# Kernel optimization log

Measured on AMD Instinct MI355X. Metric: run time of the kernel, lower is better.

The kernel has to match this reference:

```python
import jax, jax.numpy as jnp
import numpy as np

B, S, D, H = 2, 2048, 1024, 16
DK = D // H


def setup_inputs() -> dict:
    key = jax.random.key(0)
    ks = jax.random.split(key, 12)
    scale = 1.0 / np.sqrt(D)
    inp = {
        "Q": jax.random.normal(ks[0], (B, S, D), jnp.float32),
        "K": jax.random.normal(ks[1], (B, S, D), jnp.float32),
        "V": jax.random.normal(ks[2], (B, S, D), jnp.float32),
        # causal mask, broadcast over batch: [B, S, S]
        "mask": jnp.broadcast_to(jnp.tril(jnp.ones((S, S), jnp.bool_)), (B, S, S)),
        "WQ_w": jax.random.normal(ks[3], (D, D), jnp.float32) * scale,
        "WQ_b": jnp.zeros((D,), jnp.float32),
        "WK_w": jax.random.normal(ks[4], (D, D), jnp.float32) * scale,
        "WK_b": jnp.zeros((D,), jnp.float32),
        "WV_w": jax.random.normal(ks[5], (D, D), jnp.float32) * scale,
        "WV_b": jnp.zeros((D,), jnp.float32),
        "WO_w": jax.random.normal(ks[6], (D, D), jnp.float32) * scale,
        "WO_b": jnp.zeros((D,), jnp.float32),
    }
    return inp


def reference(Q, K, V, mask, WQ_w, WQ_b, WK_w, WK_b, WV_w, WV_b, WO_w, WO_b):
    # Linear projections (torch Linear: x @ W.T + b), split heads -> [B,H,S,DK]
    def proj(x, w, b):
        return (x @ w.T + b).reshape(B, S, H, DK).transpose(0, 2, 1, 3)

    q = proj(Q, WQ_w, WQ_b)
    k = proj(K, WK_w, WK_b)
    v = proj(V, WV_w, WV_b)

    scores = jnp.einsum("bhqd,bhkd->bhqk", q, k) / jnp.sqrt(jnp.asarray(DK, q.dtype))
    scores = jnp.where(mask[:, None, :, :], scores, -jnp.inf)
    attn = jax.nn.softmax(scores, axis=-1)  # dropout is identity in eval mode

    out = jnp.einsum("bhqk,bhkd->bhqd", attn, v)
    out = out.transpose(0, 2, 1, 3).reshape(B, S, D)
    out = out @ WO_w.T + WO_b
    return (out, attn)
```

## Files before the change

### kernel.cpp

```cpp
#include <hip/hip_runtime.h>

#define S_LEN 2048
#define DMODEL 1024
#define NHEAD 16
#define DKH 64
#define BATCH 2

typedef __bf16 bf16_t;
typedef __bf16 bf16x8 __attribute__((ext_vector_type(8)));
typedef __bf16 bf16x4 __attribute__((ext_vector_type(4)));
typedef float f32x4 __attribute__((ext_vector_type(4)));

__device__ __forceinline__ void gload16(const bf16_t* g, bf16_t* l) {
  __builtin_amdgcn_global_load_lds(
      (const __attribute__((address_space(1))) unsigned int*)g,
      (__attribute__((address_space(3))) unsigned int*)l,
      16, 0, 0);
}

__global__ void cvt_all(const float* __restrict__ Q, const float* __restrict__ K,
                        const float* __restrict__ V, const float* __restrict__ WQ,
                        const float* __restrict__ WK, const float* __restrict__ WV,
                        const float* __restrict__ WO, bf16_t* __restrict__ dst) {
  const int i = blockIdx.x * 256 + threadIdx.x;
  const float* src;
  int off;
  if (i < 1572864) {
    const int seg = i >> 19;
    off = i & 524287;
    src = (seg == 0) ? Q : ((seg == 1) ? K : V);
  } else {
    const int j = i - 1572864;
    const int seg = j >> 17;
    off = j & 131071;
    src = (seg == 0) ? WQ : ((seg == 1) ? WK : ((seg == 2) ? WV : WO));
  }
  f32x4 a = *(const f32x4*)(src + (size_t)off * 8);
  f32x4 b = *(const f32x4*)(src + (size_t)off * 8 + 4);
  bf16x8 v;
#pragma unroll
  for (int j = 0; j < 4; ++j) { v[j] = (bf16_t)a[j]; v[4 + j] = (bf16_t)b[j]; }
  *(bf16x8*)(dst + (size_t)i * 8) = v;
}

struct GOp {
  const bf16_t* A;
  const bf16_t* W;
  const float* bias;
  char* out;
  int emode;
};

#define GM 4096
#define GN 1024
#define GK 1024
#define BM 128
#define BN 128
#define BK 64

__launch_bounds__(256, 3)
__global__ void gemm_bf16(GOp op0, GOp op1, GOp op2) {
  GOp op = (blockIdx.z == 0) ? op0 : ((blockIdx.z == 1) ? op1 : op2);
  const int n0 = blockIdx.x * BN;
  const int m0 = blockIdx.y * BM;
  const int t = threadIdx.x;
  const int w = t >> 6;
  const int l = t & 63;
  const int wr = w >> 1, wc = w & 1;
  const int lg = l >> 4, ll = l & 15;
  const int sr = l >> 3;
  const int sc = l & 7;

  __shared__ __align__(16) bf16_t Asm[BM * BK];
  __shared__ __align__(16) bf16_t Bsm[BM * BK];

  f32x4 acc[4][4] = {};

  for (int kt = 0; kt < GK / BK; ++kt) {
    __syncthreads();
#pragma unroll
    for (int i = 0; i < 4; ++i) {
      const int rbase = i * 32 + (w << 3);
      const int row = rbase + sr;
      const int gc = (sc ^ (row & 7)) << 3;
      gload16(op.A + (size_t)(m0 + row) * GK + kt * BK + gc, &Asm[rbase * BK]);
      gload16(op.W + (size_t)(n0 + row) * GK + kt * BK + gc, &Bsm[rbase * BK]);
    }
    __syncthreads();

    bf16x8 af[4][2], bfr[4][2];
#pragma unroll
    for (int mi = 0; mi < 4; ++mi) {
      const int row = wr * 64 + mi * 16 + ll;
      af[mi][0] = *(const bf16x8*)&Asm[row * BK + ((lg ^ (row & 7)) << 3)];
      af[mi][1] = *(const bf16x8*)&Asm[row * BK + (((4 + lg) ^ (row & 7)) << 3)];
    }
#pragma unroll
    for (int ni = 0; ni < 4; ++ni) {
      const int row = wc * 64 + ni * 16 + ll;
      bfr[ni][0] = *(const bf16x8*)&Bsm[row * BK + ((lg ^ (row & 7)) << 3)];
      bfr[ni][1] = *(const bf16x8*)&Bsm[row * BK + (((4 + lg) ^ (row & 7)) << 3)];
    }
#pragma unroll
    for (int mi = 0; mi < 4; ++mi)
#pragma unroll
      for (int ni = 0; ni < 4; ++ni) {
        acc[mi][ni] = __builtin_amdgcn_mfma_f32_16x16x32_bf16(af[mi][0], bfr[ni][0], acc[mi][ni], 0, 0, 0);
        acc[mi][ni] = __builtin_amdgcn_mfma_f32_16x16x32_bf16(af[mi][1], bfr[ni][1], acc[mi][ni], 0, 0, 0);
      }
  }

#pragma unroll
  for (int mi = 0; mi < 4; ++mi) {
#pragma unroll
    for (int ni = 0; ni < 4; ++ni) {
      const int col = n0 + wc * 64 + ni * 16 + ll;
      const int rbase = m0 + wr * 64 + mi * 16 + (lg << 2);
      const float bval = op.bias[col];
      f32x4 v = acc[mi][ni];
      if (op.emode == 0) {
        bf16_t* o = (bf16_t*)op.out;
#pragma unroll
        for (int r = 0; r < 4; ++r)
          o[(size_t)(rbase + r) * GN + col] = (bf16_t)(v[r] + bval);
      } else {
        const int hh = col >> 6, dd = col & 63;
        const int bb = rbase >> 11, ss = rbase & (S_LEN - 1);
        bf16_t* o = (bf16_t*)op.out + (((size_t)bb * NHEAD + hh) * DKH + dd) * S_LEN + ss;
        bf16x4 pk;
#pragma unroll
        for (int r = 0; r < 4; ++r) pk[r] = (bf16_t)(v[r] + bval);
        *(bf16x4*)o = pk;
      }
    }
  }
}

__launch_bounds__(256, 4)
__global__ void gemm_out64(const bf16_t* __restrict__ A, const bf16_t* __restrict__ W,
                           const float* __restrict__ bias, float* __restrict__ out) {
  const int n0 = blockIdx.x * 128;
  const int m0 = blockIdx.y * 64;
  const int t = threadIdx.x;
  const int w = t >> 6;
  const int l = t & 63;
  const int wr = w >> 1, wc = w & 1;
  const int lg = l >> 4, ll = l & 15;
  const int sr = l >> 3;
  const int sc = l & 7;

  __shared__ __align__(16) bf16_t Asm[64 * BK];
  __shared__ __align__(16) bf16_t Bsm[128 * BK];

  f32x4 acc[2][4] = {};

  for (int kt = 0; kt < GK / BK; ++kt) {
    __syncthreads();
    {
#pragma unroll
      for (int i = 0; i < 2; ++i) {
        const int rbase = i * 32 + (w << 3);
        const int row = rbase + sr;
        const int gc = (sc ^ (row & 7)) << 3;
        gload16(A + (size_t)(m0 + row) * GK + kt * BK + gc, &Asm[rbase * BK]);
      }
#pragma unroll
      for (int i = 0; i < 4; ++i) {
        const int rbase = i * 32 + (w << 3);
        const int row = rbase + sr;
        const int gc = (sc ^ (row & 7)) << 3;
        gload16(W + (size_t)(n0 + row) * GK + kt * BK + gc, &Bsm[rbase * BK]);
      }
    }
    __syncthreads();

    bf16x8 af[2][2], bfr[4][2];
#pragma unroll
    for (int mi = 0; mi < 2; ++mi) {
      const int row = wr * 32 + mi * 16 + ll;
      af[mi][0] = *(const bf16x8*)&Asm[row * BK + ((lg ^ (row & 7)) << 3)];
      af[mi][1] = *(const bf16x8*)&Asm[row * BK + (((4 + lg) ^ (row & 7)) << 3)];
    }
#pragma unroll
    for (int ni = 0; ni < 4; ++ni) {
      const int row = wc * 64 + ni * 16 + ll;
      bfr[ni][0] = *(const bf16x8*)&Bsm[row * BK + ((lg ^ (row & 7)) << 3)];
      bfr[ni][1] = *(const bf16x8*)&Bsm[row * BK + (((4 + lg) ^ (row & 7)) << 3)];
    }
#pragma unroll
    for (int mi = 0; mi < 2; ++mi)
#pragma unroll
      for (int ni = 0; ni < 4; ++ni) {
        acc[mi][ni] = __builtin_amdgcn_mfma_f32_16x16x32_bf16(af[mi][0], bfr[ni][0], acc[mi][ni], 0, 0, 0);
        acc[mi][ni] = __builtin_amdgcn_mfma_f32_16x16x32_bf16(af[mi][1], bfr[ni][1], acc[mi][ni], 0, 0, 0);
      }
  }

#pragma unroll
  for (int mi = 0; mi < 2; ++mi) {
#pragma unroll
    for (int ni = 0; ni < 4; ++ni) {
      const int col = n0 + wc * 64 + ni * 16 + ll;
      const int rbase = m0 + wr * 32 + mi * 16 + (lg << 2);
      const float bval = bias[col];
      f32x4 v = acc[mi][ni];
#pragma unroll
      for (int r = 0; r < 4; ++r)
        out[(size_t)(rbase + r) * GN + col] = v[r] + bval;
    }
  }
}

__launch_bounds__(256, 2)
__global__ void attn2(const bf16_t* __restrict__ qp, const bf16_t* __restrict__ kp,
                      const bf16_t* __restrict__ vT, float* __restrict__ attn_out,
                      bf16_t* __restrict__ ctx) {
  const int raw = blockIdx.x;
  const int wg = (raw & 7) * 64 + (raw >> 3);
  const int bh = wg >> 4;
  const int pr = wg & 15;
  const int b = bh >> 4, h = bh & 15;
  const int flip = (raw >> 8) & 1;

  __shared__ __align__(16) bf16_t Qs[64 * 64];
  __shared__ __align__(16) bf16_t Ks[2][128 * 64];
  __shared__ __align__(16) bf16_t Vs[2][2][64 * 64];
  __shared__ __align__(16) bf16_t Pt[4][16 * 64];
  float* rinvS = (float*)&Pt[0][0];

  const int t = threadIdx.x;
  const int w = t >> 6;
  const int l = t & 63;
  const int lg = l >> 4;
  const int ll = l & 15;
  const int sr = l >> 3;
  const int sc = l & 7;

  const bf16_t* kbh = kp + (size_t)b * S_LEN * DMODEL + h * DKH;
  const bf16_t* vbh = vT + (size_t)bh * DKH * S_LEN;

#define KV_STAGE128(bu, ktt)                                                              \
  {                                                                                       \
    _Pragma("unroll") for (int i = 0; i < 4; ++i) {                                       \
      const int rbase = i * 32 + (w << 3);                                                \
      const int row = rbase + sr;                                                         \
      const int gc = (sc ^ (row & 7)) << 3;                                               \
      gload16(kbh + (size_t)((ktt) * 128 + row) * DMODEL + gc, &Ks[bu][rbase * 64]);      \
    }                                                                                     \
    _Pragma("unroll") for (int i = 0; i < 2; ++i) {                                       \
      const int rbase = i * 32 + (w << 3);                                                \
      const int row = rbase + sr;                                                         \
      const int gc = (sc ^ (row & 7)) << 3;                                               \
      gload16(vbh + (size_t)row * S_LEN + (ktt) * 128 + gc, &Vs[bu][0][rbase * 64]);      \
      gload16(vbh + (size_t)row * S_LEN + (ktt) * 128 + 64 + gc, &Vs[bu][1][rbase * 64]); \
    }                                                                                     \
  }

#define K_STAGE(bu, kt)                                                            \
  {                                                                                \
    _Pragma("unroll") for (int i = 0; i < 2; ++i) {                                \
      const int rbase = i * 32 + (w << 3);                                         \
      const int row = rbase + sr;                                                  \
      const int gc = (sc ^ (row & 7)) << 3;                                        \
      gload16(kbh + (size_t)((kt) * 64 + row) * DMODEL + gc, &Ks[bu][rbase * 64]); \
    }                                                                              \
  }

  for (int half = 0; half < 2; ++half) {
    const int qt = (half ^ flip) ? (31 - pr) : pr;
    const int q0 = qt * 64;
    const int nktt = (qt + 2) >> 1;

    __syncthreads();
#pragma unroll
    for (int i = 0; i < 2; ++i) {
      const int rbase = i * 32 + (w << 3);
      const int row = rbase + sr;
      const int gc = (sc ^ (row & 7)) << 3;
      gload16(qp + (size_t)(b * S_LEN + q0 + row) * DMODEL + h * DKH + gc, &Qs[rbase * 64]);
    }
    KV_STAGE128(0, 0);
    __syncthreads();

    bf16x8 qf0, qf1;
    {
      const int row = w * 16 + ll;
      qf0 = *(const bf16x8*)&Qs[row * 64 + ((lg ^ (row & 7)) << 3)];
      qf1 = *(const bf16x8*)&Qs[row * 64 + (((4 + lg) ^ (row & 7)) << 3)];
    }

    f32x4 oacc[4] = {};
    float sums[4] = {0.f, 0.f, 0.f, 0.f};
    const int qrow_base = q0 + w * 16 + (lg << 2);

    int cur = 0;
    for (int ktt = 0; ktt < nktt; ++ktt) {
      if (ktt + 1 < nktt) KV_STAGE128(cur ^ 1, ktt + 1);

      __builtin_amdgcn_s_setprio(1);
#pragma unroll
      for (int s = 0; s < 2; ++s) {
        const int kk = 2 * ktt + s;
        if (kk <= qt) {
          const bool diag = (kk == qt);
#pragma unroll
          for (int cb = 0; cb < 4; ++cb) {
            const int lr = s * 64 + cb * 16 + ll;
            bf16x8 kf0 = *(const bf16x8*)&Ks[cur][lr * 64 + ((lg ^ (lr & 7)) << 3)];
            bf16x8 kf1 = *(const bf16x8*)&Ks[cur][lr * 64 + (((4 + lg) ^ (lr & 7)) << 3)];
            f32x4 a = {0.f, 0.f, 0.f, 0.f};
            a = __builtin_amdgcn_mfma_f32_16x16x32_bf16(qf0, kf0, a, 0, 0, 0);
            a = __builtin_amdgcn_mfma_f32_16x16x32_bf16(qf1, kf1, a, 0, 0, 0);
            const int gcol = kk * 64 + cb * 16 + ll;
            if (diag) {
#pragma unroll
              for (int r = 0; r < 4; ++r) {
                const float e = (gcol <= qrow_base + r) ? __expf(a[r] * 0.125f) : 0.0f;
                sums[r] += e;
                const int ql = (lg << 2) + r;
                const int k = cb * 16 + ll;
                *(bf16_t*)((char*)&Pt[w][0] + ql * 128 + (((k >> 3) ^ (ql & 7)) << 4) + ((k & 7) << 1)) = (bf16_t)e;
              }
            } else {
#pragma unroll
              for (int r = 0; r < 4; ++r) {
                const float e = __expf(a[r] * 0.125f);
                sums[r] += e;
                const int ql = (lg << 2) + r;
                const int k = cb * 16 + ll;
                *(bf16_t*)((char*)&Pt[w][0] + ql * 128 + (((k >> 3) ^ (ql & 7)) << 4) + ((k & 7) << 1)) = (bf16_t)e;
              }
            }
          }
          bf16x8 pa0 = *(const bf16x8*)((char*)&Pt[w][0] + ll * 128 + ((lg ^ (ll & 7)) << 4));
          bf16x8 pa1 = *(const bf16x8*)((char*)&Pt[w][0] + ll * 128 + (((4 + lg) ^ (ll & 7)) << 4));
#pragma unroll
          for (int db = 0; db < 4; ++db) {
            const int drow = db * 16 + ll;
            bf16x8 vf0 = *(const bf16x8*)&Vs[cur][s][drow * 64 + ((lg ^ (drow & 7)) << 3)];
            bf16x8 vf1 = *(const bf16x8*)&Vs[cur][s][drow * 64 + (((4 + lg) ^ (drow & 7)) << 3)];
            oacc[db] = __builtin_amdgcn_mfma_f32_16x16x32_bf16(pa0, vf0, oacc[db], 0, 0, 0);
            oacc[db] = __builtin_amdgcn_mfma_f32_16x16x32_bf16(pa1, vf1, oacc[db], 0, 0, 0);
          }
        }
      }
      __builtin_amdgcn_s_setprio(0);
      __syncthreads();
      cur ^= 1;
    }

    float rinv[4];
#pragma unroll
    for (int r = 0; r < 4; ++r) {
      float s = sums[r];
      s += __shfl_xor(s, 1);
      s += __shfl_xor(s, 2);
      s += __shfl_xor(s, 4);
      s += __shfl_xor(s, 8);
      rinv[r] = 1.0f / s;
    }
    if (ll == 0) {
#pragma unroll
      for (int r = 0; r < 4; ++r) rinvS[w * 16 + (lg << 2) + r] = rinv[r];
    }

    K_STAGE(0, 0);

#pragma unroll
    for (int db = 0; db < 4; ++db)
#pragma unroll
      for (int r = 0; r < 4; ++r) {
        const int grow = q0 + w * 16 + (lg << 2) + r;
        ctx[(size_t)(b * S_LEN + grow) * DMODEL + h * DKH + db * 16 + ll] = (bf16_t)(oacc[db][r] * rinv[r]);
      }
    __syncthreads();

    const float rv = rinvS[w * 16 + ll];
    float* arow = attn_out + ((size_t)bh * S_LEN + q0) * S_LEN;

    for (int kt = qt + 1; kt < 32; ++kt) {
      f32x4 z = {0.f, 0.f, 0.f, 0.f};
#pragma unroll
      for (int j = 0; j < 4; ++j) {
        const int row = w * 16 + (lg << 2) + j;
        *(f32x4*)(arow + (size_t)row * S_LEN + kt * 64 + (ll << 2)) = z;
      }
    }

    const int qrow_sw = q0 + w * 16 + ll;
    int cur2 = 0;
    for (int kt = 0; kt <= qt; ++kt) {
      if (kt + 1 <= qt) K_STAGE(cur2 ^ 1, kt + 1);

      const bool diag = (kt == qt);
#pragma unroll
      for (int i = 0; i < 4; ++i) {
        const int krow = i * 16 + ll;
        bf16x8 kf0 = *(const bf16x8*)&Ks[cur2][krow * 64 + ((lg ^ (krow & 7)) << 3)];
        bf16x8 kf1 = *(const bf16x8*)&Ks[cur2][krow * 64 + (((4 + lg) ^ (krow & 7)) << 3)];
        f32x4 a = {0.f, 0.f, 0.f, 0.f};
        a = __builtin_amdgcn_mfma_f32_16x16x32_bf16(kf0, qf0, a, 0, 0, 0);
        a = __builtin_amdgcn_mfma_f32_16x16x32_bf16(kf1, qf1, a, 0, 0, 0);
        const int kbase = kt * 64 + i * 16 + (lg << 2);
        f32x4 o;
        if (diag) {
#pragma unroll
          for (int r = 0; r < 4; ++r)
            o[r] = (kbase + r <= qrow_sw) ? __expf(a[r] * 0.125f) * rv : 0.0f;
        } else {
#pragma unroll
          for (int r = 0; r < 4; ++r) o[r] = __expf(a[r] * 0.125f) * rv;
        }
        *(f32x4*)(arow + (size_t)(w * 16 + ll) * S_LEN + kbase) = o;
      }
      __syncthreads();
      cur2 ^= 1;
    }
  }
#undef KV_STAGE128
#undef K_STAGE
}

extern "C" void kernel_launch(void* const* d_in, const int* in_sizes, int n_in,
                              void* d_out, int out_size, void* d_ws, size_t ws_size,
                              hipStream_t stream) {
  const float* Q   = (const float*)d_in[0];
  const float* K   = (const float*)d_in[1];
  const float* V   = (const float*)d_in[2];
  const float* WQw = (const float*)d_in[4];
  const float* WQb = (const float*)d_in[5];
  const float* WKw = (const float*)d_in[6];
  const float* WKb = (const float*)d_in[7];
  const float* WVw = (const float*)d_in[8];
  const float* WVb = (const float*)d_in[9];
  const float* WOw = (const float*)d_in[10];
  const float* WOb = (const float*)d_in[11];

  char* ws = (char*)d_ws;
  bf16_t* qb  = (bf16_t*)(ws);
  bf16_t* kb  = (bf16_t*)(ws + (size_t)( 8 << 20));
  bf16_t* vb  = (bf16_t*)(ws + (size_t)(16 << 20));
  bf16_t* wq  = (bf16_t*)(ws + (size_t)(24 << 20));
  bf16_t* wk  = (bf16_t*)(ws + (size_t)(26 << 20));
  bf16_t* wv  = (bf16_t*)(ws + (size_t)(28 << 20));
  bf16_t* wo  = (bf16_t*)(ws + (size_t)(30 << 20));
  bf16_t* qp  = (bf16_t*)(ws + (size_t)(32 << 20));
  bf16_t* kp  = (bf16_t*)(ws + (size_t)(40 << 20));
  bf16_t* vT  = (bf16_t*)(ws + (size_t)(48 << 20));
  bf16_t* ctx = (bf16_t*)(ws + (size_t)(56 << 20));

  float* out_main = (float*)d_out;
  float* attn_out = out_main + (size_t)BATCH * S_LEN * DMODEL;

  cvt_all<<<dim3(8192), 256, 0, stream>>>(Q, K, V, WQw, WKw, WVw, WOw, (bf16_t*)ws);

  GOp opq{qb, wq, WQb, (char*)qp, 0};
  GOp opk{kb, wk, WKb, (char*)kp, 0};
  GOp opv{vb, wv, WVb, (char*)vT, 1};
  gemm_bf16<<<dim3(8, 32, 3), 256, 0, stream>>>(opq, opk, opv);

  attn2<<<dim3(512), 256, 0, stream>>>(qp, kp, vT, attn_out, ctx);

  gemm_out64<<<dim3(8, 64), 256, 0, stream>>>(ctx, wo, WOb, out_main);
}
```

Before: 213.8 us.

## Split attention into one query tile per block with smaller LDS for higher occupancy

The attention kernel stops processing two paired query tiles per block and gives each block a single 64-row query tile, doubling the grid to 1024 blocks with a zigzag mapping across (b,h) for load balance. K/V staging shrinks from 128-key to 64-key tiles, and the P scratch reuses the Q shared buffer, cutting LDS so launch bounds can request 4 blocks per CU. The aim is more resident waves to hide latency and less tail imbalance. In exchange there are more barriers per key, Q is reloaded per block, and lower register budgets could cause spills.

```diff
diff --git a/kernel.cpp b/kernel.cpp
--- a/kernel.cpp
+++ b/kernel.cpp
@@ -156,21 +156,19 @@
 
   for (int kt = 0; kt < GK / BK; ++kt) {
     __syncthreads();
-    {
-#pragma unroll
-      for (int i = 0; i < 2; ++i) {
-        const int rbase = i * 32 + (w << 3);
-        const int row = rbase + sr;
-        const int gc = (sc ^ (row & 7)) << 3;
-        gload16(A + (size_t)(m0 + row) * GK + kt * BK + gc, &Asm[rbase * BK]);
-      }
-#pragma unroll
-      for (int i = 0; i < 4; ++i) {
-        const int rbase = i * 32 + (w << 3);
-        const int row = rbase + sr;
-        const int gc = (sc ^ (row & 7)) << 3;
-        gload16(W + (size_t)(n0 + row) * GK + kt * BK + gc, &Bsm[rbase * BK]);
-      }
+#pragma unroll
+    for (int i = 0; i < 2; ++i) {
+      const int rbase = i * 32 + (w << 3);
+      const int row = rbase + sr;
+      const int gc = (sc ^ (row & 7)) << 3;
+      gload16(A + (size_t)(m0 + row) * GK + kt * BK + gc, &Asm[rbase * BK]);
+    }
+#pragma unroll
+    for (int i = 0; i < 4; ++i) {
+      const int rbase = i * 32 + (w << 3);
+      const int row = rbase + sr;
+      const int gc = (sc ^ (row & 7)) << 3;
+      gload16(W + (size_t)(n0 + row) * GK + kt * BK + gc, &Bsm[rbase * BK]);
     }
     __syncthreads();
 
@@ -211,22 +209,23 @@
   }
 }
 
-__launch_bounds__(256, 2)
-__global__ void attn2(const bf16_t* __restrict__ qp, const bf16_t* __restrict__ kp,
+__launch_bounds__(256, 4)
+__global__ void attn4(const bf16_t* __restrict__ qp, const bf16_t* __restrict__ kp,
                       const bf16_t* __restrict__ vT, float* __restrict__ attn_out,
                       bf16_t* __restrict__ ctx) {
   const int raw = blockIdx.x;
-  const int wg = (raw & 7) * 64 + (raw >> 3);
-  const int bh = wg >> 4;
-  const int pr = wg & 15;
+  const int wg = (raw & 7) * 128 + (raw >> 3);
+  const int bh = wg >> 5;
+  const int i5 = wg & 31;
+  const int zig = (i5 & 1) ? (31 - (i5 >> 1)) : (i5 >> 1);
+  const int qt = (bh & 1) ? (31 - zig) : zig;
   const int b = bh >> 4, h = bh & 15;
-  const int flip = (raw >> 8) & 1;
+  const int q0 = qt * 64;
+  const int nkt = qt + 1;
 
   __shared__ __align__(16) bf16_t Qs[64 * 64];
-  __shared__ __align__(16) bf16_t Ks[2][128 * 64];
-  __shared__ __align__(16) bf16_t Vs[2][2][64 * 64];
-  __shared__ __align__(16) bf16_t Pt[4][16 * 64];
-  float* rinvS = (float*)&Pt[0][0];
+  __shared__ __align__(16) bf16_t Ks[2][64 * 64];
+  __shared__ __align__(16) bf16_t Vs[2][64 * 64];
 
   const int t = threadIdx.x;
   const int w = t >> 6;
@@ -236,188 +235,173 @@
   const int sr = l >> 3;
   const int sc = l & 7;
 
+  char* PtW = (char*)Qs + (w << 11);
+  float* rinvS = (float*)Qs;
+
   const bf16_t* kbh = kp + (size_t)b * S_LEN * DMODEL + h * DKH;
   const bf16_t* vbh = vT + (size_t)bh * DKH * S_LEN;
 
-#define KV_STAGE128(bu, ktt)                                                              \
-  {                                                                                       \
-    _Pragma("unroll") for (int i = 0; i < 4; ++i) {                                       \
-      const int rbase = i * 32 + (w << 3);                                                \
-      const int row = rbase + sr;                                                         \
-      const int gc = (sc ^ (row & 7)) << 3;                                               \
-      gload16(kbh + (size_t)((ktt) * 128 + row) * DMODEL + gc, &Ks[bu][rbase * 64]);      \
-    }                                                                                     \
-    _Pragma("unroll") for (int i = 0; i < 2; ++i) {                                       \
-      const int rbase = i * 32 + (w << 3);                                                \
-      const int row = rbase + sr;                                                         \
-      const int gc = (sc ^ (row & 7)) << 3;                                               \
-      gload16(vbh + (size_t)row * S_LEN + (ktt) * 128 + gc, &Vs[bu][0][rbase * 64]);      \
-      gload16(vbh + (size_t)row * S_LEN + (ktt) * 128 + 64 + gc, &Vs[bu][1][rbase * 64]); \
-    }                                                                                     \
-  }
-
-#define K_STAGE(bu, kt)                                                            \
-  {                                                                                \
-    _Pragma("unroll") for (int i = 0; i < 2; ++i) {                                \
-      const int rbase = i * 32 + (w << 3);                                         \
-      const int row = rbase + sr;                                                  \
-      const int gc = (sc ^ (row & 7)) << 3;                                        \
-      gload16(kbh + (size_t)((kt) * 64 + row) * DMODEL + gc, &Ks[bu][rbase * 64]); \
-    }                                                                              \
-  }
-
-  for (int half = 0; half < 2; ++half) {
-    const int qt = (half ^ flip) ? (31 - pr) : pr;
-    const int q0 = qt * 64;
-    const int nktt = (qt + 2) >> 1;
-
-    __syncthreads();
-#pragma unroll
-    for (int i = 0; i < 2; ++i) {
-      const int rbase = i * 32 + (w << 3);
-      const int row = rbase + sr;
-      const int gc = (sc ^ (row & 7)) << 3;
-      gload16(qp + (size_t)(b * S_LEN + q0 + row) * DMODEL + h * DKH + gc, &Qs[rbase * 64]);
-    }
-    KV_STAGE128(0, 0);
-    __syncthreads();
-
-    bf16x8 qf0, qf1;
-    {
-      const int row = w * 16 + ll;
-      qf0 = *(const bf16x8*)&Qs[row * 64 + ((lg ^ (row & 7)) << 3)];
-      qf1 = *(const bf16x8*)&Qs[row * 64 + (((4 + lg) ^ (row & 7)) << 3)];
-    }
-
-    f32x4 oacc[4] = {};
-    float sums[4] = {0.f, 0.f, 0.f, 0.f};
-    const int qrow_base = q0 + w * 16 + (lg << 2);
-
-    int cur = 0;
-    for (int ktt = 0; ktt < nktt; ++ktt) {
-      if (ktt + 1 < nktt) KV_STAGE128(cur ^ 1, ktt + 1);
-
-      __builtin_amdgcn_s_setprio(1);
-#pragma unroll
-      for (int s = 0; s < 2; ++s) {
-        const int kk = 2 * ktt + s;
-        if (kk <= qt) {
-          const bool diag = (kk == qt);
-#pragma unroll
-          for (int cb = 0; cb < 4; ++cb) {
-            const int lr = s * 64 + cb * 16 + ll;
-            bf16x8 kf0 = *(const bf16x8*)&Ks[cur][lr * 64 + ((lg ^ (lr & 7)) << 3)];
-            bf16x8 kf1 = *(const bf16x8*)&Ks[cur][lr * 64 + (((4 + lg) ^ (lr & 7)) << 3)];
-            f32x4 a = {0.f, 0.f, 0.f, 0.f};
-            a = __builtin_amdgcn_mfma_f32_16x16x32_bf16(qf0, kf0, a, 0, 0, 0);
-            a = __builtin_amdgcn_mfma_f32_16x16x32_bf16(qf1, kf1, a, 0, 0, 0);
-            const int gcol = kk * 64 + cb * 16 + ll;
-            if (diag) {
-#pragma unroll
-              for (int r = 0; r < 4; ++r) {
-                const float e = (gcol <= qrow_base + r) ? __expf(a[r] * 0.125f) : 0.0f;
-                sums[r] += e;
-                const int ql = (lg << 2) + r;
-                const int k = cb * 16 + ll;
-                *(bf16_t*)((char*)&Pt[w][0] + ql * 128 + (((k >> 3) ^ (ql & 7)) << 4) + ((k & 7) << 1)) = (bf16_t)e;
-              }
-            } else {
-#pragma unroll
-              for (int r = 0; r < 4; ++r) {
-                const float e = __expf(a[r] * 0.125f);
-                sums[r] += e;
-                const int ql = (lg << 2) + r;
-                const int k = cb * 16 + ll;
-                *(bf16_t*)((char*)&Pt[w][0] + ql * 128 + (((k >> 3) ^ (ql & 7)) << 4) + ((k & 7) << 1)) = (bf16_t)e;
-              }
-            }
-          }
-          bf16x8 pa0 = *(const bf16x8*)((char*)&Pt[w][0] + ll * 128 + ((lg ^ (ll & 7)) << 4));
-          bf16x8 pa1 = *(const bf16x8*)((char*)&Pt[w][0] + ll * 128 + (((4 + lg) ^ (ll & 7)) << 4));
-#pragma unroll
-          for (int db = 0; db < 4; ++db) {
-            const int drow = db * 16 + ll;
-            bf16x8 vf0 = *(const bf16x8*)&Vs[cur][s][drow * 64 + ((lg ^ (drow & 7)) << 3)];
-            bf16x8 vf1 = *(const bf16x8*)&Vs[cur][s][drow * 64 + (((4 + lg) ^ (drow & 7)) << 3)];
-            oacc[db] = __builtin_amdgcn_mfma_f32_16x16x32_bf16(pa0, vf0, oacc[db], 0, 0, 0);
-            oacc[db] = __builtin_amdgcn_mfma_f32_16x16x32_bf16(pa1, vf1, oacc[db], 0, 0, 0);
-          }
+#define KV_STAGE(bu, kt_)                                                           \
+  {                                                                                 \
+    _Pragma("unroll") for (int i = 0; i < 2; ++i) {                                 \
+      const int rbase = i * 32 + (w << 3);                                          \
+      const int row = rbase + sr;                                                   \
+      const int gc = (sc ^ (row & 7)) << 3;                                         \
+      gload16(kbh + (size_t)((kt_) * 64 + row) * DMODEL + gc, &Ks[bu][rbase * 64]); \
+      gload16(vbh + (size_t)row * S_LEN + (kt_) * 64 + gc, &Vs[bu][rbase * 64]);    \
+    }                                                                               \
+  }
+
+#define K_STAGE(bu, kt_)                                                            \
+  {                                                                                 \
+    _Pragma("unroll") for (int i = 0; i < 2; ++i) {                                 \
+      const int rbase = i * 32 + (w << 3);                                          \
+      const int row = rbase + sr;                                                   \
+      const int gc = (sc ^ (row & 7)) << 3;                                         \
+      gload16(kbh + (size_t)((kt_) * 64 + row) * DMODEL + gc, &Ks[bu][rbase * 64]); \
+    }                                                                               \
+  }
+
+#pragma unroll
+  for (int i = 0; i < 2; ++i) {
+    const int rbase = i * 32 + (w << 3);
+    const int row = rbase + sr;
+    const int gc = (sc ^ (row & 7)) << 3;
+    gload16(qp + (size_t)(b * S_LEN + q0 + row) * DMODEL + h * DKH + gc, &Qs[rbase * 64]);
+  }
+  KV_STAGE(0, 0);
+  __syncthreads();
+
+  bf16x8 qf0, qf1;
+  {
+    const int row = w * 16 + ll;
+    qf0 = *(const bf16x8*)&Qs[row * 64 + ((lg ^ (row & 7)) << 3)];
+    qf1 = *(const bf16x8*)&Qs[row * 64 + (((4 + lg) ^ (row & 7)) << 3)];
+  }
+  __syncthreads();
+
+  f32x4 oacc[4] = {};
+  float sums[4] = {0.f, 0.f, 0.f, 0.f};
+  const int qrow_base = q0 + w * 16 + (lg << 2);
+
+  int cur = 0;
+  for (int kt = 0; kt < nkt; ++kt) {
+    if (kt + 1 < nkt) KV_STAGE(cur ^ 1, kt + 1);
+
+    const bool diag = (kt == qt);
+    __builtin_amdgcn_s_setprio(1);
+#pragma unroll
+    for (int cb = 0; cb < 4; ++cb) {
+      const int krow = cb * 16 + ll;
+      bf16x8 kf0 = *(const bf16x8*)&Ks[cur][krow * 64 + ((lg ^ (krow & 7)) << 3)];
+      bf16x8 kf1 = *(const bf16x8*)&Ks[cur][krow * 64 + (((4 + lg) ^ (krow & 7)) << 3)];
+      f32x4 a = {0.f, 0.f, 0.f, 0.f};
+      a = __builtin_amdgcn_mfma_f32_16x16x32_bf16(qf0, kf0, a, 0, 0, 0);
+      a = __builtin_amdgcn_mfma_f32_16x16x32_bf16(qf1, kf1, a, 0, 0, 0);
+      const int gcol = kt * 64 + krow;
+      if (diag) {
+#pragma unroll
+        for (int r = 0; r < 4; ++r) {
+          const float e = (gcol <= qrow_base + r) ? __expf(a[r] * 0.125f) : 0.0f;
+          sums[r] += e;
+          const int ql = (lg << 2) + r;
+          const int k = cb * 16 + ll;
+          *(bf16_t*)(PtW + ql * 128 + (((k >> 3) ^ (ql & 7)) << 4) + ((k & 7) << 1)) = (bf16_t)e;
+        }
+      } else {
+#pragma unroll
+        for (int r = 0; r < 4; ++r) {
+          const float e = __expf(a[r] * 0.125f);
+          sums[r] += e;
+          const int ql = (lg << 2) + r;
+          const int k = cb * 16 + ll;
+          *(bf16_t*)(PtW + ql * 128 + (((k >> 3) ^ (ql & 7)) << 4) + ((k & 7) << 1)) = (bf16_t)e;
         }
       }
-      __builtin_amdgcn_s_setprio(0);
-      __syncthreads();
-      cur ^= 1;
-    }
-
-    float rinv[4];
+    }
+    bf16x8 pa0 = *(const bf16x8*)(PtW + ll * 128 + ((lg ^ (ll & 7)) << 4));
+    bf16x8 pa1 = *(const bf16x8*)(PtW + ll * 128 + (((4 + lg) ^ (ll & 7)) << 4));
+#pragma unroll
+    for (int db = 0; db < 4; ++db) {
+      const int drow = db * 16 + ll;
+      bf16x8 vf0 = *(const bf16x8*)&Vs[cur][drow * 64 + ((lg ^ (drow & 7)) << 3)];
+      bf16x8 vf1 = *(const bf16x8*)&Vs[cur][drow * 64 + (((4 + lg) ^ (drow & 7)) << 3)];
+      oacc[db] = __builtin_amdgcn_mfma_f32_16x16x32_bf16(pa0, vf0, oacc[db], 0, 0, 0);
+      oacc[db] = __builtin_amdgcn_mfma_f32_16x16x32_bf16(pa1, vf1, oacc[db], 0, 0, 0);
+    }
+    __builtin_amdgcn_s_setprio(0);
+    __syncthreads();
+    cur ^= 1;
+  }
+
+  float rinv[4];
+#pragma unroll
+  for (int r = 0; r < 4; ++r) {
+    float s = sums[r];
+    s += __shfl_xor(s, 1);
+    s += __shfl_xor(s, 2);
+    s += __shfl_xor(s, 4);
+    s += __shfl_xor(s, 8);
+    rinv[r] = 1.0f / s;
+  }
+  if (ll == 0) {
+#pragma unroll
+    for (int r = 0; r < 4; ++r) rinvS[w * 16 + (lg << 2) + r] = rinv[r];
+  }
+
+  K_STAGE(0, 0);
+
+#pragma unroll
+  for (int db = 0; db < 4; ++db)
 #pragma unroll
     for (int r = 0; r < 4; ++r) {
-      float s = sums[r];
-      s += __shfl_xor(s, 1);
-      s += __shfl_xor(s, 2);
-      s += __shfl_xor(s, 4);
-      s += __shfl_xor(s, 8);
-      rinv[r] = 1.0f / s;
-    }
-    if (ll == 0) {
-#pragma unroll
-      for (int r = 0; r < 4; ++r) rinvS[w * 16 + (lg << 2) + r] = rinv[r];
-    }
-
-    K_STAGE(0, 0);
-
-#pragma unroll
-    for (int db = 0; db < 4; ++db)
-#pragma unroll
-      for (int r = 0; r < 4; ++r) {
-        const int grow = q0 + w * 16 + (lg << 2) + r;
-        ctx[(size_t)(b * S_LEN + grow) * DMODEL + h * DKH + db * 16 + ll] = (bf16_t)(oacc[db][r] * rinv[r]);
+      const int grow = q0 + w * 16 + (lg << 2) + r;
+      ctx[(size_t)(b * S_LEN + grow) * DMODEL + h * DKH + db * 16 + ll] = (bf16_t)(oacc[db][r] * rinv[r]);
+    }
+  __syncthreads();
+
+  const float rv = rinvS[w * 16 + ll];
+  float* arow = attn_out + ((size_t)bh * S_LEN + q0) * S_LEN;
+
+  for (int kt = qt + 1; kt < 32; ++kt) {
+    f32x4 z = {0.f, 0.f, 0.f, 0.f};
+#pragma unroll
+    for (int j = 0; j < 4; ++j) {
+      const int row = w * 16 + (lg << 2) + j;
+      *(f32x4*)(arow + (size_t)row * S_LEN + kt * 64 + (ll << 2)) = z;
+    }
+  }
+
+  const int qrow_sw = q0 + w * 16 + ll;
+  int cur2 = 0;
+  for (int kt = 0; kt <= qt; ++kt) {
+    if (kt + 1 <= qt) K_STAGE(cur2 ^ 1, kt + 1);
+
+    const bool diag = (kt == qt);
+#pragma unroll
+    for (int i = 0; i < 4; ++i) {
+      const int krow = i * 16 + ll;
+      bf16x8 kf0 = *(const bf16x8*)&Ks[cur2][krow * 64 + ((lg ^ (krow & 7)) << 3)];
+      bf16x8 kf1 = *(const bf16x8*)&Ks[cur2][krow * 64 + (((4 + lg) ^ (krow & 7)) << 3)];
+      f32x4 a = {0.f, 0.f, 0.f, 0.f};
+      a = __builtin_amdgcn_mfma_f32_16x16x32_bf16(kf0, qf0, a, 0, 0, 0);
+      a = __builtin_amdgcn_mfma_f32_16x16x32_bf16(kf1, qf1, a, 0, 0, 0);
+      const int kbase = kt * 64 + i * 16 + (lg << 2);
+      f32x4 o;
+      if (diag) {
+#pragma unroll
+        for (int r = 0; r < 4; ++r)
+          o[r] = (kbase + r <= qrow_sw) ? __expf(a[r] * 0.125f) * rv : 0.0f;
+      } else {
+#pragma unroll
+        for (int r = 0; r < 4; ++r) o[r] = __expf(a[r] * 0.125f) * rv;
       }
-    __syncthreads();
-
-    const float rv = rinvS[w * 16 + ll];
-    float* arow = attn_out + ((size_t)bh * S_LEN + q0) * S_LEN;
-
-    for (int kt = qt + 1; kt < 32; ++kt) {
-      f32x4 z = {0.f, 0.f, 0.f, 0.f};
-#pragma unroll
-      for (int j = 0; j < 4; ++j) {
-        const int row = w * 16 + (lg << 2) + j;
-        *(f32x4*)(arow + (size_t)row * S_LEN + kt * 64 + (ll << 2)) = z;
-      }
-    }
-
-    const int qrow_sw = q0 + w * 16 + ll;
-    int cur2 = 0;
-    for (int kt = 0; kt <= qt; ++kt) {
-      if (kt + 1 <= qt) K_STAGE(cur2 ^ 1, kt + 1);
-
-      const bool diag = (kt == qt);
-#pragma unroll
-      for (int i = 0; i < 4; ++i) {
-        const int krow = i * 16 + ll;
-        bf16x8 kf0 = *(const bf16x8*)&Ks[cur2][krow * 64 + ((lg ^ (krow & 7)) << 3)];
-        bf16x8 kf1 = *(const bf16x8*)&Ks[cur2][krow * 64 + (((4 + lg) ^ (krow & 7)) << 3)];
-        f32x4 a = {0.f, 0.f, 0.f, 0.f};
-        a = __builtin_amdgcn_mfma_f32_16x16x32_bf16(kf0, qf0, a, 0, 0, 0);
-        a = __builtin_amdgcn_mfma_f32_16x16x32_bf16(kf1, qf1, a, 0, 0, 0);
-        const int kbase = kt * 64 + i * 16 + (lg << 2);
-        f32x4 o;
-        if (diag) {
-#pragma unroll
-          for (int r = 0; r < 4; ++r)
-            o[r] = (kbase + r <= qrow_sw) ? __expf(a[r] * 0.125f) * rv : 0.0f;
-        } else {
-#pragma unroll
-          for (int r = 0; r < 4; ++r) o[r] = __expf(a[r] * 0.125f) * rv;
-        }
-        *(f32x4*)(arow + (size_t)(w * 16 + ll) * S_LEN + kbase) = o;
-      }
-      __syncthreads();
-      cur2 ^= 1;
-    }
-  }
-#undef KV_STAGE128
+      *(f32x4*)(arow + (size_t)(w * 16 + ll) * S_LEN + kbase) = o;
+    }
+    __syncthreads();
+    cur2 ^= 1;
+  }
+#undef KV_STAGE
 #undef K_STAGE
 }
 
@@ -459,7 +443,7 @@
   GOp opv{vb, wv, WVb, (char*)vT, 1};
   gemm_bf16<<<dim3(8, 32, 3), 256, 0, stream>>>(opq, opk, opv);
 
-  attn2<<<dim3(512), 256, 0, stream>>>(qp, kp, vT, attn_out, ctx);
+  attn4<<<dim3(1024), 256, 0, stream>>>(qp, kp, vT, attn_out, ctx);
 
   gemm_out64<<<dim3(8, 64), 256, 0, stream>>>(ctx, wo, WOb, out_main);
 }
```

Measured after the change: 232.8 us. +8.9%, slower.

## Batch K tiles in groups of four in attention-prob write pass

Applied to the files above, without the earlier changes.

Replaces the separate shared arrays in the attention kernel with one flat buffer and reuses the K/V region as eight 64-row K buffers. In the second pass, which recomputes and writes the normalized attention probabilities, K tiles are now loaded four at a time with double-buffered groups, so each sync covers four tiles instead of one. This cuts barrier count and deepens prefetch on a pass dominated by stores, at the cost of more LDS traffic in flight per group.

```diff
diff --git a/kernel.cpp b/kernel.cpp
--- a/kernel.cpp
+++ b/kernel.cpp
@@ -156,21 +156,19 @@
 
   for (int kt = 0; kt < GK / BK; ++kt) {
     __syncthreads();
-    {
-#pragma unroll
-      for (int i = 0; i < 2; ++i) {
-        const int rbase = i * 32 + (w << 3);
-        const int row = rbase + sr;
-        const int gc = (sc ^ (row & 7)) << 3;
-        gload16(A + (size_t)(m0 + row) * GK + kt * BK + gc, &Asm[rbase * BK]);
-      }
-#pragma unroll
-      for (int i = 0; i < 4; ++i) {
-        const int rbase = i * 32 + (w << 3);
-        const int row = rbase + sr;
-        const int gc = (sc ^ (row & 7)) << 3;
-        gload16(W + (size_t)(n0 + row) * GK + kt * BK + gc, &Bsm[rbase * BK]);
-      }
+#pragma unroll
+    for (int i = 0; i < 2; ++i) {
+      const int rbase = i * 32 + (w << 3);
+      const int row = rbase + sr;
+      const int gc = (sc ^ (row & 7)) << 3;
+      gload16(A + (size_t)(m0 + row) * GK + kt * BK + gc, &Asm[rbase * BK]);
+    }
+#pragma unroll
+    for (int i = 0; i < 4; ++i) {
+      const int rbase = i * 32 + (w << 3);
+      const int row = rbase + sr;
+      const int gc = (sc ^ (row & 7)) << 3;
+      gload16(W + (size_t)(n0 + row) * GK + kt * BK + gc, &Bsm[rbase * BK]);
     }
     __syncthreads();
 
@@ -222,11 +220,13 @@
   const int b = bh >> 4, h = bh & 15;
   const int flip = (raw >> 8) & 1;
 
-  __shared__ __align__(16) bf16_t Qs[64 * 64];
-  __shared__ __align__(16) bf16_t Ks[2][128 * 64];
-  __shared__ __align__(16) bf16_t Vs[2][2][64 * 64];
-  __shared__ __align__(16) bf16_t Pt[4][16 * 64];
-  float* rinvS = (float*)&Pt[0][0];
+  __shared__ __align__(16) bf16_t SMEM[40960];
+  bf16_t* Qs = SMEM;
+  bf16_t* KsB = SMEM + 4096;
+  bf16_t* VsB = SMEM + 20480;
+  bf16_t* PtB = SMEM + 36864;
+  bf16_t* KB = SMEM + 4096;
+  float* rinvS = (float*)PtB;
 
   const int t = threadIdx.x;
   const int w = t >> 6;
@@ -235,35 +235,37 @@
   const int ll = l & 15;
   const int sr = l >> 3;
   const int sc = l & 7;
+  char* PtW = (char*)PtB + (w << 11);
 
   const bf16_t* kbh = kp + (size_t)b * S_LEN * DMODEL + h * DKH;
   const bf16_t* vbh = vT + (size_t)bh * DKH * S_LEN;
 
-#define KV_STAGE128(bu, ktt)                                                              \
-  {                                                                                       \
-    _Pragma("unroll") for (int i = 0; i < 4; ++i) {                                       \
-      const int rbase = i * 32 + (w << 3);                                                \
-      const int row = rbase + sr;                                                         \
-      const int gc = (sc ^ (row & 7)) << 3;                                               \
-      gload16(kbh + (size_t)((ktt) * 128 + row) * DMODEL + gc, &Ks[bu][rbase * 64]);      \
-    }                                                                                     \
-    _Pragma("unroll") for (int i = 0; i < 2; ++i) {                                       \
-      const int rbase = i * 32 + (w << 3);                                                \
-      const int row = rbase + sr;                                                         \
-      const int gc = (sc ^ (row & 7)) << 3;                                               \
-      gload16(vbh + (size_t)row * S_LEN + (ktt) * 128 + gc, &Vs[bu][0][rbase * 64]);      \
-      gload16(vbh + (size_t)row * S_LEN + (ktt) * 128 + 64 + gc, &Vs[bu][1][rbase * 64]); \
-    }                                                                                     \
-  }
-
-#define K_STAGE(bu, kt)                                                            \
-  {                                                                                \
-    _Pragma("unroll") for (int i = 0; i < 2; ++i) {                                \
-      const int rbase = i * 32 + (w << 3);                                         \
-      const int row = rbase + sr;                                                  \
-      const int gc = (sc ^ (row & 7)) << 3;                                        \
-      gload16(kbh + (size_t)((kt) * 64 + row) * DMODEL + gc, &Ks[bu][rbase * 64]); \
-    }                                                                              \
+#define KV_STAGE128(bu, ktt)                                                                   \
+  {                                                                                            \
+    _Pragma("unroll") for (int i = 0; i < 4; ++i) {                                            \
+      const int rbase = i * 32 + (w << 3);                                                     \
+      const int row = rbase + sr;                                                              \
+      const int gc = (sc ^ (row & 7)) << 3;                                                    \
+      gload16(kbh + (size_t)((ktt) * 128 + row) * DMODEL + gc, KsB + (bu) * 8192 + rbase * 64);\
+    }                                                                                          \
+    _Pragma("unroll") for (int i = 0; i < 2; ++i) {                                            \
+      const int rbase = i * 32 + (w << 3);                                                     \
+      const int row = rbase + sr;                                                              \
+      const int gc = (sc ^ (row & 7)) << 3;                                                    \
+      gload16(vbh + (size_t)row * S_LEN + (ktt) * 128 + gc, VsB + (bu) * 8192 + rbase * 64);   \
+      gload16(vbh + (size_t)row * S_LEN + (ktt) * 128 + 64 + gc,                               \
+              VsB + (bu) * 8192 + 4096 + rbase * 64);                                          \
+    }                                                                                          \
+  }
+
+#define K_STAGE_KB(idx, kt_)                                                                   \
+  {                                                                                            \
+    _Pragma("unroll") for (int i = 0; i < 2; ++i) {                                            \
+      const int rbase = i * 32 + (w << 3);                                                     \
+      const int row = rbase + sr;                                                              \
+      const int gc = (sc ^ (row & 7)) << 3;                                                    \
+      gload16(kbh + (size_t)((kt_) * 64 + row) * DMODEL + gc, KB + (idx) * 4096 + rbase * 64); \
+    }                                                                                          \
   }
 
   for (int half = 0; half < 2; ++half) {
@@ -277,7 +279,7 @@
       const int rbase = i * 32 + (w << 3);
       const int row = rbase + sr;
       const int gc = (sc ^ (row & 7)) << 3;
-      gload16(qp + (size_t)(b * S_LEN + q0 + row) * DMODEL + h * DKH + gc, &Qs[rbase * 64]);
+      gload16(qp + (size_t)(b * S_LEN + q0 + row) * DMODEL + h * DKH + gc, Qs + rbase * 64);
     }
     KV_STAGE128(0, 0);
     __syncthreads();
@@ -306,8 +308,8 @@
 #pragma unroll
           for (int cb = 0; cb < 4; ++cb) {
             const int lr = s * 64 + cb * 16 + ll;
-            bf16x8 kf0 = *(const bf16x8*)&Ks[cur][lr * 64 + ((lg ^ (lr & 7)) << 3)];
-            bf16x8 kf1 = *(const bf16x8*)&Ks[cur][lr * 64 + (((4 + lg) ^ (lr & 7)) << 3)];
+            bf16x8 kf0 = *(const bf16x8*)&KsB[cur * 8192 + lr * 64 + ((lg ^ (lr & 7)) << 3)];
+            bf16x8 kf1 = *(const bf16x8*)&KsB[cur * 8192 + lr * 64 + (((4 + lg) ^ (lr & 7)) << 3)];
             f32x4 a = {0.f, 0.f, 0.f, 0.f};
             a = __builtin_amdgcn_mfma_f32_16x16x32_bf16(qf0, kf0, a, 0, 0, 0);
             a = __builtin_amdgcn_mfma_f32_16x16x32_bf16(qf1, kf1, a, 0, 0, 0);
@@ -319,7 +321,7 @@
                 sums[r] += e;
                 const int ql = (lg << 2) + r;
                 const int k = cb * 16 + ll;
-                *(bf16_t*)((char*)&Pt[w][0] + ql * 128 + (((k >> 3) ^ (ql & 7)) << 4) + ((k & 7) << 1)) = (bf16_t)e;
+                *(bf16_t*)(PtW + ql * 128 + (((k >> 3) ^ (ql & 7)) << 4) + ((k & 7) << 1)) = (bf16_t)e;
               }
             } else {
 #pragma unroll
@@ -328,17 +330,17 @@
                 sums[r] += e;
                 const int ql = (lg << 2) + r;
                 const int k = cb * 16 + ll;
-                *(bf16_t*)((char*)&Pt[w][0] + ql * 128 + (((k >> 3) ^ (ql & 7)) << 4) + ((k & 7) << 1)) = (bf16_t)e;
+                *(bf16_t*)(PtW + ql * 128 + (((k >> 3) ^ (ql & 7)) << 4) + ((k & 7) << 1)) = (bf16_t)e;
               }
             }
           }
-          bf16x8 pa0 = *(const bf16x8*)((char*)&Pt[w][0] + ll * 128 + ((lg ^ (ll & 7)) << 4));
-          bf16x8 pa1 = *(const bf16x8*)((char*)&Pt[w][0] + ll * 128 + (((4 + lg) ^ (ll & 7)) << 4));
+          bf16x8 pa0 = *(const bf16x8*)(PtW + ll * 128 + ((lg ^ (ll & 7)) << 4));
+          bf16x8 pa1 = *(const bf16x8*)(PtW + ll * 128 + (((4 + lg) ^ (ll & 7)) << 4));
 #pragma unroll
           for (int db = 0; db < 4; ++db) {
             const int drow = db * 16 + ll;
-            bf16x8 vf0 = *(const bf16x8*)&Vs[cur][s][drow * 64 + ((lg ^ (drow & 7)) << 3)];
-            bf16x8 vf1 = *(const bf16x8*)&Vs[cur][s][drow * 64 + (((4 + lg) ^ (drow & 7)) << 3)];
+            bf16x8 vf0 = *(const bf16x8*)&VsB[cur * 8192 + s * 4096 + drow * 64 + ((lg ^ (drow & 7)) << 3)];
+            bf16x8 vf1 = *(const bf16x8*)&VsB[cur * 8192 + s * 4096 + drow * 64 + (((4 + lg) ^ (drow & 7)) << 3)];
             oacc[db] = __builtin_amdgcn_mfma_f32_16x16x32_bf16(pa0, vf0, oacc[db], 0, 0, 0);
             oacc[db] = __builtin_amdgcn_mfma_f32_16x16x32_bf16(pa1, vf1, oacc[db], 0, 0, 0);
           }
@@ -364,7 +366,9 @@
       for (int r = 0; r < 4; ++r) rinvS[w * 16 + (lg << 2) + r] = rinv[r];
     }
 
-    K_STAGE(0, 0);
+#pragma unroll
+    for (int j = 0; j < 4; ++j)
+      if (j <= qt) K_STAGE_KB(j, j);
 
 #pragma unroll
     for (int db = 0; db < 4; ++db)
@@ -388,37 +392,48 @@
     }
 
     const int qrow_sw = q0 + w * 16 + ll;
-    int cur2 = 0;
-    for (int kt = 0; kt <= qt; ++kt) {
-      if (kt + 1 <= qt) K_STAGE(cur2 ^ 1, kt + 1);
-
-      const bool diag = (kt == qt);
-#pragma unroll
-      for (int i = 0; i < 4; ++i) {
-        const int krow = i * 16 + ll;
-        bf16x8 kf0 = *(const bf16x8*)&Ks[cur2][krow * 64 + ((lg ^ (krow & 7)) << 3)];
-        bf16x8 kf1 = *(const bf16x8*)&Ks[cur2][krow * 64 + (((4 + lg) ^ (krow & 7)) << 3)];
-        f32x4 a = {0.f, 0.f, 0.f, 0.f};
-        a = __builtin_amdgcn_mfma_f32_16x16x32_bf16(kf0, qf0, a, 0, 0, 0);
-        a = __builtin_amdgcn_mfma_f32_16x16x32_bf16(kf1, qf1, a, 0, 0, 0);
-        const int kbase = kt * 64 + i * 16 + (lg << 2);
-        f32x4 o;
-        if (diag) {
-#pragma unroll
-          for (int r = 0; r < 4; ++r)
-            o[r] = (kbase + r <= qrow_sw) ? __expf(a[r] * 0.125f) * rv : 0.0f;
-        } else {
-#pragma unroll
-          for (int r = 0; r < 4; ++r) o[r] = __expf(a[r] * 0.125f) * rv;
+    const int ngrp = (qt + 4) >> 2;
+    for (int g = 0; g < ngrp; ++g) {
+      const int nb = ((g + 1) & 1) << 2;
+#pragma unroll
+      for (int j = 0; j < 4; ++j) {
+        const int kt2 = (g + 1) * 4 + j;
+        if (kt2 <= qt) K_STAGE_KB(nb + j, kt2);
+      }
+      const int cb2 = (g & 1) << 2;
+#pragma unroll
+      for (int j = 0; j < 4; ++j) {
+        const int kt = g * 4 + j;
+        if (kt <= qt) {
+          const bool diag = (kt == qt);
+          const bf16_t* Kbuf = KB + (cb2 + j) * 4096;
+#pragma unroll
+          for (int i = 0; i < 4; ++i) {
+            const int krow = i * 16 + ll;
+            bf16x8 kf0 = *(const bf16x8*)&Kbuf[krow * 64 + ((lg ^ (krow & 7)) << 3)];
+            bf16x8 kf1 = *(const bf16x8*)&Kbuf[krow * 64 + (((4 + lg) ^ (krow & 7)) << 3)];
+            f32x4 a = {0.f, 0.f, 0.f, 0.f};
+            a = __builtin_amdgcn_mfma_f32_16x16x32_bf16(kf0, qf0, a, 0, 0, 0);
+            a = __builtin_amdgcn_mfma_f32_16x16x32_bf16(kf1, qf1, a, 0, 0, 0);
+            const int kbase = kt * 64 + i * 16 + (lg << 2);
+            f32x4 o;
+            if (diag) {
+#pragma unroll
+              for (int r = 0; r < 4; ++r)
+                o[r] = (kbase + r <= qrow_sw) ? __expf(a[r] * 0.125f) * rv : 0.0f;
+            } else {
+#pragma unroll
+              for (int r = 0; r < 4; ++r) o[r] = __expf(a[r] * 0.125f) * rv;
+            }
+            *(f32x4*)(arow + (size_t)(w * 16 + ll) * S_LEN + kbase) = o;
+          }
         }
-        *(f32x4*)(arow + (size_t)(w * 16 + ll) * S_LEN + kbase) = o;
       }
       __syncthreads();
-      cur2 ^= 1;
     }
   }
 #undef KV_STAGE128
-#undef K_STAGE
+#undef K_STAGE_KB
 }
 
 extern "C" void kernel_launch(void* const* d_in, const int* in_sizes, int n_in,
```

New measurement: 211.1 us (median of 2 runs). Within noise of the previous version (-1.3%).
